# Performance work log

Measured on AMD Instinct MI355X. Metric: run time of the kernel, lower is better.

The kernel has to match this reference:

```python
import jax, jax.numpy as jnp
import numpy as np

B, S, D, H, C, E, V = 8, 2048, 1024, 512, 256, 64, 64


def setup_inputs() -> dict:
    key = jax.random.key(0)
    ks = jax.random.split(key, 40)
    ri = lambda i, hi: jax.random.randint(ks[i], (B, S), 0, hi).astype(jnp.int32)
    p = lambda i, shape: (jax.random.normal(ks[i], shape, jnp.float32) * 0.02)
    inp = {
        'h_x': jax.random.normal(ks[0], (B, S, D), jnp.float32),
        'h_y': jax.random.normal(ks[1], (B, S, D), jnp.float32),
        'x_mask': jnp.ones((B, S), jnp.int32),
        'y_mask': jnp.ones((B, S), jnp.int32),
        'src_token_dense_mask': ri(2, 2), 'src_token_sparse_mask': ri(3, 2),
        'src_token_inarc_type': ri(4, V), 'src_token_arc_head': ri(5, S),
        'src_token_depth': ri(6, 16), 'src_word_inarc_type': ri(7, V),
        'src_word_inarc_type_mask': ri(8, 2),
        'tgt_token_dense_mask': ri(9, 2), 'tgt_token_sparse_mask': ri(10, 2),
        'tgt_token_inarc_type': ri(11, V), 'tgt_token_arc_head': ri(12, S),
        'tgt_token_depth': ri(13, 16), 'tgt_word_inarc_type': ri(14, V),
        'tgt_word_inarc_type_mask': ri(15, 2),
        # src MLP [D->H->C], tgt MLP [D->H->C]
        'W1s': p(16, (D, H)), 'b1s': jnp.zeros((H,), jnp.float32),
        'W2s': p(17, (H, C)), 'b2s': jnp.zeros((C,), jnp.float32),
        'W1t': p(18, (D, H)), 'b1t': jnp.zeros((H,), jnp.float32),
        'W2t': p(19, (H, C)), 'b2t': jnp.zeros((C,), jnp.float32),
        # inarc edge embedding + GeneralConv params
        'emb': p(20, (V, E)),
        'W_msg': p(21, (C, C)), 'b_msg': jnp.zeros((C,), jnp.float32),
        'W_edge': p(22, (E, C)),
        'att': p(23, (C,)),
        'W_self': p(24, (C, C)), 'b_self': jnp.zeros((C,), jnp.float32),
        # axis_feature MLP [C->C]
        'Wf': p(25, (C, C)), 'bf': jnp.zeros((C,), jnp.float32),
    }
    return inp


def _mlp(h, W1, b1, W2, b2):
    return jax.nn.leaky_relu(h @ W1 + b1) @ W2 + b2


def _graph_side(h, dense_m, sparse_m, arc_head, word_type, word_mask,
                W1, b1, W2, b2, emb, W_msg, b_msg, W_edge, att, W_self, b_self, Wf, bf):
    Bn, Sn, _ = h.shape
    x = _mlp(h, W1, b1, W2, b2)                      # [B,S,C]
    N = Bn * Sn
    Cn = x.shape[-1]
    xg = x.reshape(N, Cn)                            # debatch -> nodes
    off = (jnp.arange(Bn, dtype=jnp.int32) * Sn)[:, None]
    src = (arc_head + off).reshape(N)                # global head index per token
    dst = jnp.arange(N, dtype=jnp.int32)             # one in-edge per token
    valid = (sparse_m * dense_m).reshape(N).astype(x.dtype)
    ef = emb[(word_type * word_mask).reshape(N)]     # [N,E] edge embeddings
    # GeneralConv: directed message with edge features + additive attention
    m = xg[src] @ W_msg + b_msg + ef @ W_edge        # [N,C] messages
    hd = xg @ W_msg + b_msg                          # dst-side term for attention
    logit = jax.nn.leaky_relu(((m + hd) * att).sum(-1))
    logit = jnp.where(valid > 0, logit, -1e9)
    emax = jax.ops.segment_max(logit, dst, num_segments=N)
    ex = jnp.exp(logit - emax[dst]) * valid
    den = jax.ops.segment_sum(ex, dst, num_segments=N)
    alpha = ex / (den[dst] + 1e-16)                  # softmax per destination node
    agg = jax.ops.segment_sum(m * alpha[:, None], dst, num_segments=N)
    out = xg @ W_self + b_self + agg                 # skip_linear
    out = out / jnp.maximum(jnp.linalg.norm(out, axis=-1, keepdims=True), 1e-12)
    r = out.reshape(Bn, Sn, Cn).mean(axis=1, keepdims=True)  # FeatureRepr mean
    return r @ Wf + bf                               # [B,1,C]


def reference(h_x, x_mask, src_token_dense_mask, src_token_sparse_mask,
              src_token_inarc_type, src_token_arc_head, src_token_depth,
              src_word_inarc_type, src_word_inarc_type_mask,
              h_y, y_mask, tgt_token_dense_mask, tgt_token_sparse_mask,
              tgt_token_inarc_type, tgt_token_arc_head, tgt_token_depth,
              tgt_word_inarc_type, tgt_word_inarc_type_mask,
              W1s, b1s, W2s, b2s, W1t, b1t, W2t, b2t,
              emb, W_msg, b_msg, W_edge, att, W_self, b_self, Wf, bf):
    src_repr = _graph_side(h_x, src_token_dense_mask, src_token_sparse_mask,
                           src_token_arc_head, src_word_inarc_type, src_word_inarc_type_mask,
                           W1s, b1s, W2s, b2s, emb, W_msg, b_msg, W_edge, att,
                           W_self, b_self, Wf, bf)
    tgt_repr = _graph_side(h_y, tgt_token_dense_mask, tgt_token_sparse_mask,
                           tgt_token_arc_head, tgt_word_inarc_type, tgt_word_inarc_type_mask,
                           W1t, b1t, W2t, b2t, emb, W_msg, b_msg, W_edge, att,
                           W_self, b_self, Wf, bf)
    return (src_repr, tgt_repr)
```

## Files before the change

kernel.cpp:

```cpp
#include <hip/hip_runtime.h>
#include <stdint.h>

#define SEQ   2048
#define NNODE 16384

typedef short  short8  __attribute__((ext_vector_type(8)));
typedef float  float4v __attribute__((ext_vector_type(4)));
typedef unsigned short u16;
typedef unsigned short u16x8 __attribute__((ext_vector_type(8)));
typedef short  short4v __attribute__((ext_vector_type(4)));

__device__ __forceinline__ float b2f(u16 u) {
    union { unsigned int i; float f; } x; x.i = ((unsigned int)u) << 16; return x.f;
}
__device__ __forceinline__ u16 f2b(float f) {
    union { float f; unsigned int i; } x; x.f = f;
    unsigned int u = x.i;
    unsigned int r = (u + 0x7fffu + ((u >> 16) & 1u)) >> 16;
    return (u16)r;
}

__device__ __forceinline__ void gld16(const void* g, void* l) {
    __builtin_amdgcn_global_load_lds(
        (const __attribute__((address_space(1))) void*)g,
        (__attribute__((address_space(3))) void*)l, 16, 0, 0);
}

struct GemmP {
    const u16*   A[2];
    const u16*   B[2];
    const float* bias[2];
    u16*         out[2];
};

#define PHASE(ASL, BSL, KH, STAGE, DO_VM)                                     \
    {                                                                         \
        short8 af[4], bq[4];                                                  \
        _Pragma("unroll") for (int mi = 0; mi < 4; ++mi)                      \
            af[mi] = *(const short8*)((ASL) +                                 \
                (size_t)(wm * 64 + mi * 16 + lr) * 64 +                       \
                (((KH) * 4 + lk) ^ (lr & 7)) * 8);                            \
        _Pragma("unroll") for (int ni = 0; ni < 4; ++ni)                      \
            bq[ni] = *(const short8*)((BSL) +                                 \
                (size_t)(wn * 64 + ni * 16 + lr) * 64 +                       \
                (((KH) * 4 + lk) ^ (lr & 7)) * 8);                            \
        STAGE;                                                                \
        if (DO_VM) asm volatile("s_waitcnt vmcnt(6)" ::: "memory");           \
        __builtin_amdgcn_s_barrier();                                         \
        asm volatile("s_waitcnt lgkmcnt(0)" ::: "memory");                    \
        __builtin_amdgcn_s_setprio(1);                                        \
        _Pragma("unroll") for (int mi = 0; mi < 4; ++mi)                      \
            _Pragma("unroll") for (int ni = 0; ni < 4; ++ni)                  \
                acc[mi][ni] = __builtin_amdgcn_mfma_f32_16x16x32_bf16(        \
                    af[mi], bq[ni], acc[mi][ni], 0, 0, 0);                    \
        __builtin_amdgcn_s_setprio(0);                                        \
        __builtin_amdgcn_s_barrier();                                         \
    }

template <int ACT>
__global__ __launch_bounds__(512, 2) void gemmt_k(GemmP p, int M, int N, int K) {
    __shared__ __align__(16) u16 smem[73728];

    const int z = blockIdx.z;
    const u16*   __restrict__ Ag   = p.A[z];
    const u16*   __restrict__ Bg   = p.B[z];
    const float* __restrict__ bias = p.bias[z];

    const int mt  = blockIdx.x * 256;
    const int nt  = blockIdx.y * 128;
    const int tid = threadIdx.x;
    const int l   = tid & 63;
    const int w   = tid >> 6;
    const int wm  = w >> 1;
    const int wn  = w & 1;
    const int lr  = l & 15;
    const int lk  = l >> 4;
    (void)M;

    float4v acc[4][4] = {};

    const int srow   = tid >> 3;
    const int gchunk = (tid & 7) ^ (srow & 7);

    u16* const As0 = smem;
    u16* const Bs0 = smem + 49152;

    auto stageA = [&](int k0, u16* dst) {
#pragma unroll
        for (int i = 0; i < 4; ++i)
            gld16(Ag + (size_t)(mt + srow + 64 * i) * K + k0 + gchunk * 8,
                  dst + (size_t)(tid + 512 * i) * 8);
    };
    auto stageB = [&](int k0, u16* dst) {
#pragma unroll
        for (int i = 0; i < 2; ++i)
            gld16(Bg + (size_t)(nt + srow + 64 * i) * K + k0 + gchunk * 8,
                  dst + (size_t)(tid + 512 * i) * 8);
    };

    const int NT = K >> 6;

    stageA(0, As0);       stageB(0, Bs0);
    stageA(64, As0 + 16384); stageB(64, Bs0 + 8192);
    asm volatile("s_waitcnt vmcnt(6)" ::: "memory");
    __builtin_amdgcn_s_barrier();

    int sc = 0;
    for (int T = 0; T < NT; ++T) {
        const int sc2 = (sc >= 1) ? sc - 1 : 2;
        u16* Ac = As0 + sc  * 16384;  u16* Bc = Bs0 + sc  * 8192;
        u16* A2 = As0 + sc2 * 16384;  u16* B2 = Bs0 + sc2 * 8192;
        const int k2 = (T + 2 < NT) ? (T + 2) << 6 : 0;
        PHASE(Ac, Bc, 0, stageA(k2, A2), 0)
        PHASE(Ac, Bc, 1, stageB(k2, B2), 1)
        sc = (sc == 2) ? 0 : sc + 1;
    }

    __syncthreads();

    const int er0 = lk * 4;
    float bvv[4];
#pragma unroll
    for (int ni = 0; ni < 4; ++ni) bvv[ni] = bias[nt + wn * 64 + ni * 16 + lr];
#pragma unroll
    for (int mi = 0; mi < 4; ++mi)
#pragma unroll
        for (int ni = 0; ni < 4; ++ni) {
            const int lc = wn * 64 + ni * 16 + lr;
#pragma unroll
            for (int r = 0; r < 4; ++r) {
                float v = acc[mi][ni][r] + bvv[ni];
                if (ACT) v = v > 0.f ? v : 0.01f * v;
                smem[(size_t)(wm * 64 + mi * 16 + er0 + r) * 136 + lc] = f2b(v);
            }
        }
    __syncthreads();
#pragma unroll
    for (int it = 0; it < 8; ++it) {
        const int id  = it * 512 + tid;
        const int row = id >> 4, colc = id & 15;
        u16x8 vv = *(const u16x8*)(smem + (size_t)row * 136 + colc * 8);
        *(u16x8*)(p.out[z] + (size_t)(mt + row) * N + nt + colc * 8) = vv;
    }
}

struct CvtP { const float* src[2]; u16* dst[2]; };

__global__ __launch_bounds__(256) void cvt_k(CvtP q, int n8) {
    const int side = blockIdx.y;
    const float4v* __restrict__ s = (const float4v*)q.src[side];
    u16* __restrict__ d = q.dst[side];
    for (int i = blockIdx.x * 256 + threadIdx.x; i < n8; i += gridDim.x * 256) {
        float4v a = s[2 * i], b = s[2 * i + 1];
        u16x8 r;
        r[0] = f2b(a[0]); r[1] = f2b(a[1]); r[2] = f2b(a[2]); r[3] = f2b(a[3]);
        r[4] = f2b(b[0]); r[5] = f2b(b[1]); r[6] = f2b(b[2]); r[7] = f2b(b[3]);
        *(u16x8*)(d + (size_t)i * 8) = r;
    }
}

struct TP { const float* src[6]; u16* dst[6]; int K[6]; int N[6]; };

__global__ __launch_bounds__(256) void transpose_k(TP t) {
    __shared__ float tile[64][65];
    const int m = blockIdx.y;
    const int K = t.K[m], N = t.N[m];
    const int tn = N >> 6;
    const int ntiles = (K >> 6) * tn;
    const int bid = blockIdx.x;
    if (bid >= ntiles) return;
    const int k0 = (bid / tn) * 64, n0 = (bid % tn) * 64;
    const int tid = threadIdx.x;
#pragma unroll
    for (int pass = 0; pass < 4; ++pass) {
        int kk = pass * 16 + (tid >> 4);
        int nn = (tid & 15) * 4;
        float4v v = *(const float4v*)(t.src[m] + (size_t)(k0 + kk) * N + n0 + nn);
        tile[kk][nn + 0] = v[0]; tile[kk][nn + 1] = v[1];
        tile[kk][nn + 2] = v[2]; tile[kk][nn + 3] = v[3];
    }
    __syncthreads();
    const int n = tid >> 2, kc = (tid & 3) * 16;
    u16x8 a, b;
#pragma unroll
    for (int j = 0; j < 8; ++j) {
        a[j] = f2b(tile[kc + j][n]);
        b[j] = f2b(tile[kc + 8 + j][n]);
    }
    u16* d = t.dst[m] + (size_t)(n0 + n) * K + k0 + kc;
    *(u16x8*)d = a;
    *(u16x8*)(d + 8) = b;
}

__global__ void ew_k(const float* emb, const float* W_edge, float* EW) {
    const int t = blockIdx.x, c = threadIdx.x;
    float p0 = 0.f, p1 = 0.f, p2 = 0.f, p3 = 0.f;
    for (int e = 0; e < 64; e += 4) {
        p0 += emb[t * 64 + e + 0] * W_edge[(e + 0) * 256 + c];
        p1 += emb[t * 64 + e + 1] * W_edge[(e + 1) * 256 + c];
        p2 += emb[t * 64 + e + 2] * W_edge[(e + 2) * 256 + c];
        p3 += emb[t * 64 + e + 3] * W_edge[(e + 3) * 256 + c];
    }
    EW[t * 256 + c] = (p0 + p1) + (p2 + p3);
}

struct WmP { const float* W2[2]; const float* Wmsg; const float* Wself;
             float* W23[2]; };

__global__ __launch_bounds__(512) void wmul_k(WmP q) {
    __shared__ float w2[16][256];
    const int side = blockIdx.y;
    const int k0 = blockIdx.x * 16;
    const int n = threadIdx.x;
    const float* __restrict__ W2 = q.W2[side];
    for (int i = threadIdx.x; i < 4096; i += 512)
        w2[i >> 8][i & 255] = W2[(size_t)(k0 + (i >> 8)) * 256 + (i & 255)];
    __syncthreads();
    const float* __restrict__ Wc = (n < 256) ? q.Wmsg : q.Wself;
    const int nn = n & 255;
    float acc[16] = {};
    for (int c = 0; c < 256; c += 4) {
        const float wc0 = Wc[(c + 0) * 256 + nn];
        const float wc1 = Wc[(c + 1) * 256 + nn];
        const float wc2 = Wc[(c + 2) * 256 + nn];
        const float wc3 = Wc[(c + 3) * 256 + nn];
#pragma unroll
        for (int kk = 0; kk < 16; ++kk)
            acc[kk] += w2[kk][c] * wc0 + w2[kk][c + 1] * wc1 +
                       w2[kk][c + 2] * wc2 + w2[kk][c + 3] * wc3;
    }
    for (int kk = 0; kk < 16; ++kk)
        q.W23[side][(size_t)(k0 + kk) * 512 + n] = acc[kk];
}

struct B23WP { const float* b2[2]; const float* bmsg; const float* bself;
               const float* Wmsg; const float* Wself; float* b23; };

__global__ void b23w_k(B23WP q) {
    const int side = blockIdx.x;
    const int n = threadIdx.x;
    const float* __restrict__ W = (n < 256) ? q.Wmsg : q.Wself;
    const int nn = n & 255;
    const float* __restrict__ b2 = q.b2[side];
    float p[8] = {};
    for (int c = 0; c < 256; c += 8) {
#pragma unroll
        for (int j = 0; j < 8; ++j)
            p[j] += b2[c + j] * W[(c + j) * 256 + nn];
    }
    float s = (n < 256) ? q.bmsg[nn] : q.bself[nn];
    s += ((p[0] + p[1]) + (p[2] + p[3])) + ((p[4] + p[5]) + (p[6] + p[7]));
    q.b23[side * 512 + n] = s;
}

struct EpiP {
    const u16* xcat[2];
    const int* den[2]; const int* spa[2]; const int* arc[2];
    const int* wty[2]; const int* wma[2];
    const float* EW; float* racc;
};

__global__ __launch_bounds__(256) void epi_k(EpiP p) {
    __shared__ float part[4][256];
    const int bx    = blockIdx.x;
    const int side  = bx >> 9;
    const int local = bx & 511;
    const int base  = local * 32;
    const int b     = base >> 11;
    const int tid   = threadIdx.x;
    const int w = tid >> 6, l = tid & 63;

    const u16* __restrict__ xcat = p.xcat[side];

    float4v acc = {};
    for (int j = 0; j < 8; ++j) {
        const int i     = base + w * 8 + j;
        const int valid = p.den[side][i] * p.spa[side][i];
        const int srcn  = p.arc[side][i] + (i >> 11) * SEQ;
        const int t     = p.wty[side][i] * p.wma[side][i];
        short4v xs = *(const short4v*)(xcat + (size_t)i * 512 + 256 + l * 4);
        short4v xm = *(const short4v*)(xcat + (size_t)srcn * 512 + l * 4);
        float4v ew = *(const float4v*)(p.EW + (size_t)t * 256 + l * 4);
        const float vm = valid ? 1.f : 0.f;
        float4v v;
        v[0] = b2f((u16)xs[0]) + vm * (b2f((u16)xm[0]) + ew[0]);
        v[1] = b2f((u16)xs[1]) + vm * (b2f((u16)xm[1]) + ew[1]);
        v[2] = b2f((u16)xs[2]) + vm * (b2f((u16)xm[2]) + ew[2]);
        v[3] = b2f((u16)xs[3]) + vm * (b2f((u16)xm[3]) + ew[3]);
        float ss = v[0]*v[0] + v[1]*v[1] + v[2]*v[2] + v[3]*v[3];
        for (int m = 32; m >= 1; m >>= 1) ss += __shfl_xor(ss, m, 64);
        const float rn = 1.f / fmaxf(sqrtf(ss), 1e-12f);
        acc[0] += v[0] * rn; acc[1] += v[1] * rn;
        acc[2] += v[2] * rn; acc[3] += v[3] * rn;
    }
    part[w][l * 4 + 0] = acc[0];
    part[w][l * 4 + 1] = acc[1];
    part[w][l * 4 + 2] = acc[2];
    part[w][l * 4 + 3] = acc[3];
    __syncthreads();
    const float s = part[0][tid] + part[1][tid] + part[2][tid] + part[3][tid];
    atomicAdd(p.racc + ((size_t)side * 8 + b) * 256 + tid, s);
}

__global__ void fin_k(const float* racc, const float* Wf, const float* bfv,
                      float* out) {
    __shared__ float r[256];
    const int bid = blockIdx.x;
    const int tid = threadIdx.x;
    r[tid] = racc[bid * 256 + tid] * (1.f / 2048.f);
    __syncthreads();
    float s = bfv[tid];
    for (int k = 0; k < 256; ++k)
        s += r[k] * Wf[k * 256 + tid];
    out[bid * 256 + tid] = s;
}

extern "C" void kernel_launch(void* const* d_in, const int* in_sizes, int n_in,
                              void* d_out, int out_size, void* d_ws, size_t ws_size,
                              hipStream_t stream) {
    const float* h[2]   = {(const float*)d_in[0],  (const float*)d_in[1]};
    const int* den[2]   = {(const int*)d_in[4],  (const int*)d_in[11]};
    const int* spa[2]   = {(const int*)d_in[5],  (const int*)d_in[12]};
    const int* arc[2]   = {(const int*)d_in[7],  (const int*)d_in[14]};
    const int* wty[2]   = {(const int*)d_in[9],  (const int*)d_in[16]};
    const int* wma[2]   = {(const int*)d_in[10], (const int*)d_in[17]};
    const float* W1[2]  = {(const float*)d_in[18], (const float*)d_in[22]};
    const float* b1[2]  = {(const float*)d_in[19], (const float*)d_in[23]};
    const float* W2[2]  = {(const float*)d_in[20], (const float*)d_in[24]};
    const float* b2[2]  = {(const float*)d_in[21], (const float*)d_in[25]};
    const float* emb    = (const float*)d_in[26];
    const float* Wmsg   = (const float*)d_in[27];
    const float* bmsg   = (const float*)d_in[28];
    const float* Wedge  = (const float*)d_in[29];
    const float* Wself  = (const float*)d_in[31];
    const float* bself  = (const float*)d_in[32];
    const float* Wf     = (const float*)d_in[33];
    const float* bf_    = (const float*)d_in[34];

    char* ws = (char*)d_ws;
    size_t off = 0;
    auto alloc = [&](size_t bytes) -> void* {
        void* pp = ws + off; off += (bytes + 255) & ~(size_t)255; return pp;
    };
    u16*   x1    = (u16*)  alloc(2ull * NNODE * 512 * 2);
    u16*   hb    = (u16*)  alloc(2ull * NNODE * 1024 * 2);
    u16*   xcat  = hb;
    u16*   W1T   = (u16*)  alloc(2ull * 512 * 1024 * 2);
    float* W23   = (float*)alloc(2ull * 512 * 512 * 4);
    u16*   W23T  = (u16*)  alloc(2ull * 512 * 512 * 2);
    float* EW    = (float*)alloc(64 * 256 * 4);
    float* b23   = (float*)alloc(2 * 512 * 4);
    float* racc  = (float*)alloc(2 * 8 * 256 * 4);

    CvtP cq;
    cq.src[0] = h[0]; cq.src[1] = h[1];
    cq.dst[0] = hb;   cq.dst[1] = hb + (size_t)NNODE * 1024;
    hipLaunchKernelGGL(cvt_k, dim3(2048, 2), dim3(256), 0, stream,
                       cq, NNODE * 1024 / 8);

    TP tp = {};
    tp.src[0] = W1[0]; tp.dst[0] = W1T;              tp.K[0] = 1024; tp.N[0] = 512;
    tp.src[1] = W1[1]; tp.dst[1] = W1T + 512 * 1024; tp.K[1] = 1024; tp.N[1] = 512;
    hipLaunchKernelGGL(transpose_k, dim3(128, 2), dim3(256), 0, stream, tp);
    hipLaunchKernelGGL(ew_k, dim3(64), dim3(256), 0, stream, emb, Wedge, EW);

    WmP wq;
    wq.W2[0] = W2[0]; wq.W2[1] = W2[1];
    wq.Wmsg = Wmsg; wq.Wself = Wself;
    wq.W23[0] = W23; wq.W23[1] = W23 + 512 * 512;
    hipLaunchKernelGGL(wmul_k, dim3(32, 2), dim3(512), 0, stream, wq);

    TP tp2 = {};
    tp2.src[0] = W23;            tp2.dst[0] = W23T;            tp2.K[0] = 512; tp2.N[0] = 512;
    tp2.src[1] = W23 + 512*512;  tp2.dst[1] = W23T + 512*512;  tp2.K[1] = 512; tp2.N[1] = 512;
    hipLaunchKernelGGL(transpose_k, dim3(64, 2), dim3(256), 0, stream, tp2);

    B23WP bq;
    bq.b2[0] = b2[0]; bq.b2[1] = b2[1];
    bq.bmsg = bmsg; bq.bself = bself;
    bq.Wmsg = Wmsg; bq.Wself = Wself;
    bq.b23 = b23;
    hipLaunchKernelGGL(b23w_k, dim3(2), dim3(512), 0, stream, bq);
    hipMemsetAsync(racc, 0, 2 * 8 * 256 * 4, stream);

    GemmP g1 = {};
    g1.A[0] = hb;  g1.A[1] = hb + (size_t)NNODE * 1024;
    g1.B[0] = W1T; g1.B[1] = W1T + 512 * 1024;
    g1.bias[0] = b1[0]; g1.bias[1] = b1[1];
    g1.out[0] = x1; g1.out[1] = x1 + (size_t)NNODE * 512;
    hipLaunchKernelGGL((gemmt_k<1>), dim3(64, 4, 2), dim3(512), 0, stream,
                       g1, NNODE, 512, 1024);

    GemmP g23 = {};
    g23.A[0] = x1;   g23.A[1] = x1 + (size_t)NNODE * 512;
    g23.B[0] = W23T; g23.B[1] = W23T + 512 * 512;
    g23.bias[0] = b23; g23.bias[1] = b23 + 512;
    g23.out[0] = xcat; g23.out[1] = xcat + (size_t)NNODE * 512;
    hipLaunchKernelGGL((gemmt_k<0>), dim3(64, 4, 2), dim3(512), 0, stream,
                       g23, NNODE, 512, 512);

    EpiP ep;
    ep.xcat[0] = xcat; ep.xcat[1] = xcat + (size_t)NNODE * 512;
    for (int s = 0; s < 2; ++s) {
        ep.den[s] = den[s]; ep.spa[s] = spa[s]; ep.arc[s] = arc[s];
        ep.wty[s] = wty[s]; ep.wma[s] = wma[s];
    }
    ep.EW = EW; ep.racc = racc;
    hipLaunchKernelGGL(epi_k, dim3(1024), dim3(256), 0, stream, ep);

    hipLaunchKernelGGL(fin_k, dim3(16), dim3(256), 0, stream,
                       racc, Wf, bf_, (float*)d_out);
}
```

Before: 368.5 us.

## Fuse fp32-to-bf16 input conversion into first GEMM and swizzle tile order

Removes the standalone fp32-to-bf16 conversion kernel. The first GEMM now loads fp32 activations straight into registers, converts them, and writes them to LDS, software-pipelined one tile ahead. This avoids writing and re-reading a 64MB bf16 intermediate. It also flattens the grid with a block swizzle so neighbouring blocks share B tiles, and unrolls the k-loop by two so the rotation of the triple buffer is static. The cost is higher register pressure and an A path built from VGPR loads instead of direct-to-LDS loads, which may weaken overlap in the first GEMM.

```diff
diff --git a/kernel.cpp b/kernel.cpp
--- a/kernel.cpp
+++ b/kernel.cpp
@@ -27,13 +27,17 @@
 }
 
 struct GemmP {
-    const u16*   A[2];
+    const void*  A[2];
     const u16*   B[2];
     const float* bias[2];
     u16*         out[2];
 };
 
-#define PHASE(ASL, BSL, KH, STAGE, DO_VM)                                     \
+#define NOVM
+#define VM6  asm volatile("s_waitcnt vmcnt(6)" ::: "memory");
+#define VM10 asm volatile("s_waitcnt vmcnt(10)" ::: "memory");
+
+#define PHASE(ASL, BSL, KH, STAGE, VMW)                                       \
     {                                                                         \
         short8 af[4], bq[4];                                                  \
         _Pragma("unroll") for (int mi = 0; mi < 4; ++mi)                      \
@@ -45,7 +49,7 @@
                 (size_t)(wn * 64 + ni * 16 + lr) * 64 +                       \
                 (((KH) * 4 + lk) ^ (lr & 7)) * 8);                            \
         STAGE;                                                                \
-        if (DO_VM) asm volatile("s_waitcnt vmcnt(6)" ::: "memory");           \
+        VMW                                                                   \
         __builtin_amdgcn_s_barrier();                                         \
         asm volatile("s_waitcnt lgkmcnt(0)" ::: "memory");                    \
         __builtin_amdgcn_s_setprio(1);                                        \
@@ -57,17 +61,21 @@
         __builtin_amdgcn_s_barrier();                                         \
     }
 
-template <int ACT>
+template <int ACT, int AF32>
 __global__ __launch_bounds__(512, 2) void gemmt_k(GemmP p, int M, int N, int K) {
     __shared__ __align__(16) u16 smem[73728];
 
     const int z = blockIdx.z;
-    const u16*   __restrict__ Ag   = p.A[z];
+    const u16*   __restrict__ A16  = (const u16*)p.A[z];
+    const float* __restrict__ A32  = (const float*)p.A[z];
     const u16*   __restrict__ Bg   = p.B[z];
     const float* __restrict__ bias = p.bias[z];
 
-    const int mt  = blockIdx.x * 256;
-    const int nt  = blockIdx.y * 128;
+    const int flat = blockIdx.x;
+    const int swz  = ((flat & 7) << 5) | (flat >> 3);
+    const int mt   = (swz >> 2) * 256;
+    const int nt   = (swz & 3) * 128;
+
     const int tid = threadIdx.x;
     const int l   = tid & 63;
     const int w   = tid >> 6;
@@ -78,6 +86,7 @@
     (void)M;
 
     float4v acc[4][4] = {};
+    float4v paA[8], paB[8];
 
     const int srow   = tid >> 3;
     const int gchunk = (tid & 7) ^ (srow & 7);
@@ -88,7 +97,7 @@
     auto stageA = [&](int k0, u16* dst) {
 #pragma unroll
         for (int i = 0; i < 4; ++i)
-            gld16(Ag + (size_t)(mt + srow + 64 * i) * K + k0 + gchunk * 8,
+            gld16(A16 + (size_t)(mt + srow + 64 * i) * K + k0 + gchunk * 8,
                   dst + (size_t)(tid + 512 * i) * 8);
     };
     auto stageB = [&](int k0, u16* dst) {
@@ -97,23 +106,65 @@
             gld16(Bg + (size_t)(nt + srow + 64 * i) * K + k0 + gchunk * 8,
                   dst + (size_t)(tid + 512 * i) * 8);
     };
+    auto prefA32 = [&](int k0, float4v* pa) {
+#pragma unroll
+        for (int i = 0; i < 4; ++i) {
+            const float* s = A32 + (size_t)(mt + srow + 64 * i) * K
+                                 + k0 + gchunk * 8;
+            pa[2 * i]     = *(const float4v*)s;
+            pa[2 * i + 1] = *(const float4v*)(s + 4);
+        }
+    };
+    auto cvtWrite = [&](const float4v* pa, u16* dst) {
+#pragma unroll
+        for (int i = 0; i < 4; ++i) {
+            const float4v a = pa[2 * i], b = pa[2 * i + 1];
+            u16x8 r;
+            r[0] = f2b(a[0]); r[1] = f2b(a[1]); r[2] = f2b(a[2]); r[3] = f2b(a[3]);
+            r[4] = f2b(b[0]); r[5] = f2b(b[1]); r[6] = f2b(b[2]); r[7] = f2b(b[3]);
+            *(u16x8*)(dst + (size_t)(tid + 512 * i) * 8) = r;
+        }
+    };
 
     const int NT = K >> 6;
 
-    stageA(0, As0);       stageB(0, Bs0);
-    stageA(64, As0 + 16384); stageB(64, Bs0 + 8192);
-    asm volatile("s_waitcnt vmcnt(6)" ::: "memory");
+    if constexpr (AF32) {
+        float4v p0[8];
+        prefA32(0, p0);
+        stageB(0, Bs0);
+        prefA32(64, paB);
+        stageB(64, Bs0 + 8192);
+        cvtWrite(p0, As0);
+        asm volatile("s_waitcnt vmcnt(10)" ::: "memory");
+        asm volatile("s_waitcnt lgkmcnt(0)" ::: "memory");
+    } else {
+        stageA(0, As0);          stageB(0, Bs0);
+        stageA(64, As0 + 16384); stageB(64, Bs0 + 8192);
+        asm volatile("s_waitcnt vmcnt(6)" ::: "memory");
+    }
     __builtin_amdgcn_s_barrier();
 
     int sc = 0;
-    for (int T = 0; T < NT; ++T) {
-        const int sc2 = (sc >= 1) ? sc - 1 : 2;
+    for (int T = 0; T < NT; T += 2) {
+        const int sc1 = (sc == 2) ? 0 : sc + 1;
+        const int sc2 = (sc1 == 2) ? 0 : sc1 + 1;
         u16* Ac = As0 + sc  * 16384;  u16* Bc = Bs0 + sc  * 8192;
+        u16* Ao = As0 + sc1 * 16384;  u16* Bo = Bs0 + sc1 * 8192;
         u16* A2 = As0 + sc2 * 16384;  u16* B2 = Bs0 + sc2 * 8192;
         const int k2 = (T + 2 < NT) ? (T + 2) << 6 : 0;
-        PHASE(Ac, Bc, 0, stageA(k2, A2), 0)
-        PHASE(Ac, Bc, 1, stageB(k2, B2), 1)
-        sc = (sc == 2) ? 0 : sc + 1;
+        const int k3 = (T + 3 < NT) ? (T + 3) << 6 : 0;
+        if constexpr (AF32) {
+            PHASE(Ac, Bc, 0, prefA32(k2, paA), NOVM)
+            PHASE(Ac, Bc, 1, { stageB(k2, B2); cvtWrite(paB, Ao); }, VM10)
+            PHASE(Ao, Bo, 0, prefA32(k3, paB), NOVM)
+            PHASE(Ao, Bo, 1, { stageB(k3, Bc); cvtWrite(paA, A2); }, VM10)
+        } else {
+            PHASE(Ac, Bc, 0, stageA(k2, A2), NOVM)
+            PHASE(Ac, Bc, 1, stageB(k2, B2), VM6)
+            PHASE(Ao, Bo, 0, stageA(k3, Ac), NOVM)
+            PHASE(Ao, Bo, 1, stageB(k3, Bc), VM6)
+        }
+        sc = sc2;
     }
 
     __syncthreads();
@@ -141,21 +192,6 @@
         const int row = id >> 4, colc = id & 15;
         u16x8 vv = *(const u16x8*)(smem + (size_t)row * 136 + colc * 8);
         *(u16x8*)(p.out[z] + (size_t)(mt + row) * N + nt + colc * 8) = vv;
-    }
-}
-
-struct CvtP { const float* src[2]; u16* dst[2]; };
-
-__global__ __launch_bounds__(256) void cvt_k(CvtP q, int n8) {
-    const int side = blockIdx.y;
-    const float4v* __restrict__ s = (const float4v*)q.src[side];
-    u16* __restrict__ d = q.dst[side];
-    for (int i = blockIdx.x * 256 + threadIdx.x; i < n8; i += gridDim.x * 256) {
-        float4v a = s[2 * i], b = s[2 * i + 1];
-        u16x8 r;
-        r[0] = f2b(a[0]); r[1] = f2b(a[1]); r[2] = f2b(a[2]); r[3] = f2b(a[3]);
-        r[4] = f2b(b[0]); r[5] = f2b(b[1]); r[6] = f2b(b[2]); r[7] = f2b(b[3]);
-        *(u16x8*)(d + (size_t)i * 8) = r;
     }
 }
 
@@ -343,20 +379,13 @@
         void* pp = ws + off; off += (bytes + 255) & ~(size_t)255; return pp;
     };
     u16*   x1    = (u16*)  alloc(2ull * NNODE * 512 * 2);
-    u16*   hb    = (u16*)  alloc(2ull * NNODE * 1024 * 2);
-    u16*   xcat  = hb;
+    u16*   xcat  = (u16*)  alloc(2ull * NNODE * 512 * 2);
     u16*   W1T   = (u16*)  alloc(2ull * 512 * 1024 * 2);
     float* W23   = (float*)alloc(2ull * 512 * 512 * 4);
     u16*   W23T  = (u16*)  alloc(2ull * 512 * 512 * 2);
     float* EW    = (float*)alloc(64 * 256 * 4);
     float* b23   = (float*)alloc(2 * 512 * 4);
     float* racc  = (float*)alloc(2 * 8 * 256 * 4);
-
-    CvtP cq;
-    cq.src[0] = h[0]; cq.src[1] = h[1];
-    cq.dst[0] = hb;   cq.dst[1] = hb + (size_t)NNODE * 1024;
-    hipLaunchKernelGGL(cvt_k, dim3(2048, 2), dim3(256), 0, stream,
-                       cq, NNODE * 1024 / 8);
 
     TP tp = {};
     tp.src[0] = W1[0]; tp.dst[0] = W1T;              tp.K[0] = 1024; tp.N[0] = 512;
@@ -384,11 +413,11 @@
     hipMemsetAsync(racc, 0, 2 * 8 * 256 * 4, stream);
 
     GemmP g1 = {};
-    g1.A[0] = hb;  g1.A[1] = hb + (size_t)NNODE * 1024;
-    g1.B[0] = W1T; g1.B[1] = W1T + 512 * 1024;
+    g1.A[0] = h[0]; g1.A[1] = h[1];
+    g1.B[0] = W1T;  g1.B[1] = W1T + 512 * 1024;
     g1.bias[0] = b1[0]; g1.bias[1] = b1[1];
     g1.out[0] = x1; g1.out[1] = x1 + (size_t)NNODE * 512;
-    hipLaunchKernelGGL((gemmt_k<1>), dim3(64, 4, 2), dim3(512), 0, stream,
+    hipLaunchKernelGGL((gemmt_k<1, 1>), dim3(256, 1, 2), dim3(512), 0, stream,
                        g1, NNODE, 512, 1024);
 
     GemmP g23 = {};
@@ -396,7 +425,7 @@
     g23.B[0] = W23T; g23.B[1] = W23T + 512 * 512;
     g23.bias[0] = b23; g23.bias[1] = b23 + 512;
     g23.out[0] = xcat; g23.out[1] = xcat + (size_t)NNODE * 512;
-    hipLaunchKernelGGL((gemmt_k<0>), dim3(64, 4, 2), dim3(512), 0, stream,
+    hipLaunchKernelGGL((gemmt_k<0, 0>), dim3(256, 1, 2), dim3(512), 0, stream,
                        g23, NNODE, 512, 512);
 
     EpiP ep;
```

Measured after the change: 371.1 us. About the same (+0.7%).
